# Optimization experiments

Hardware: AMD Instinct MI355X
Metric: run time of the kernel (lower is better)

Reference implementation:

```python
import jax, jax.numpy as jnp
import numpy as np

B, L, HID, NH, NB = 8, 1024, 512, 8, 8
HD = HID // NH


def setup_inputs() -> dict:
    key = jax.random.key(0)
    ks = jax.random.split(key, 12)
    s = 1.0 / np.sqrt(HID)
    x = jax.random.normal(ks[0], (B, L, HID), dtype=jnp.float32)
    time_bucket_matrix = jax.random.randint(ks[1], (B, L, L), 0, NB, dtype=jnp.int32)
    causal_mask = jnp.triu(jnp.ones((L, L), dtype=bool), k=1)  # True = masked (future)
    lens = jax.random.randint(ks[2], (B,), (7 * L) // 8, L + 1)
    padding_mask = jnp.arange(L)[None, :] >= lens[:, None]  # True = pad
    return {
        "x": x,
        "time_bucket_matrix": time_bucket_matrix,
        "causal_mask": causal_mask,
        "padding_mask": padding_mask,
        "Wq": jax.random.uniform(ks[3], (HID, HID), jnp.float32, -s, s),
        "bq": jnp.zeros((HID,), jnp.float32),
        "Wk": jax.random.uniform(ks[4], (HID, HID), jnp.float32, -s, s),
        "bk": jnp.zeros((HID,), jnp.float32),
        "Wv": jax.random.uniform(ks[5], (HID, HID), jnp.float32, -s, s),
        "bv": jnp.zeros((HID,), jnp.float32),
        "Wo": jax.random.uniform(ks[6], (HID, HID), jnp.float32, -s, s),
        "bo": jnp.zeros((HID,), jnp.float32),
        "time_emb": jax.random.normal(ks[7], (NB, NH), dtype=jnp.float32),
    }


def reference(x, time_bucket_matrix, causal_mask, padding_mask,
              Wq, bq, Wk, bk, Wv, bv, Wo, bo, time_emb):
    Bb, Ll, H = x.shape
    def heads(t):
        return t.reshape(Bb, Ll, NH, HD).transpose(0, 2, 1, 3)  # [B,NH,L,HD]
    q = heads(x @ Wq.T + bq)
    k = heads(x @ Wk.T + bk)
    v = heads(x @ Wv.T + bv)
    scores = jnp.einsum("bhqd,bhkd->bhqk", q, k) / jnp.sqrt(jnp.float32(HD))
    # per-(i,j) time-bucket bias: [B,L,L] -> [B,L,L,NH] -> [B,NH,L,L]
    t_bias = time_emb[time_bucket_matrix].transpose(0, 3, 1, 2)
    scores = scores + t_bias
    scores = jnp.where(causal_mask[None, None, :, :], -1e9, scores)
    scores = jnp.where(padding_mask[:, None, None, :], -1e9, scores)  # key pad
    w = jax.nn.softmax(scores, axis=-1)
    w = jnp.where(padding_mask[:, None, :, None], 0.0, w)  # query pad
    out = jnp.einsum("bhqk,bhkd->bhqd", w, v).transpose(0, 2, 1, 3).reshape(Bb, Ll, H)
    return out @ Wo.T + bo
```

## Files before the change

kernel.cpp:

```cpp
#include <hip/hip_runtime.h>
#include <hip/hip_bf16.h>
#include <cstdint>

#define L_SEQ 1024
#define HID_DIM 512
#define N_HEADS 8
#define HEAD_DIM 64
#define BATCH 8

typedef __attribute__((ext_vector_type(8))) short bf16x8;
typedef __attribute__((ext_vector_type(4))) float f32x4;

__device__ __forceinline__ ushort f2bf(float v) {
  __hip_bfloat16 hb = __float2bfloat16(v);
  return *(ushort*)&hb;
}

__global__ __launch_bounds__(256)
void prep_convert(const float* __restrict__ x, const float* __restrict__ Wq,
                  const float* __restrict__ Wk, const float* __restrict__ Wv,
                  const float* __restrict__ Wo, ushort* __restrict__ dst) {
  const size_t gid = (size_t)blockIdx.x * 256 + threadIdx.x;
  const size_t e = gid * 8;
  const float* src;
  size_t loc;
  if (e < 4194304) {
    src = x; loc = e;
  } else {
    const size_t r = e - 4194304;
    const int wsel = (int)(r >> 18);
    loc = r & 262143;
    src = (wsel == 0) ? Wq : (wsel == 1) ? Wk : (wsel == 2) ? Wv : Wo;
  }
  float4 v0 = *(const float4*)(src + loc);
  float4 v1 = *(const float4*)(src + loc + 4);
  ushort u[8];
  u[0] = f2bf(v0.x); u[1] = f2bf(v0.y); u[2] = f2bf(v0.z); u[3] = f2bf(v0.w);
  u[4] = f2bf(v1.x); u[5] = f2bf(v1.y); u[6] = f2bf(v1.z); u[7] = f2bf(v1.w);
  *(uint4*)(dst + e) = *(uint4*)u;
}

__global__ __launch_bounds__(256)
void lens_kernel(const uint8_t* __restrict__ pm, int* __restrict__ lens) {
  __shared__ int flag;
  __shared__ int part[256];
  const int b = blockIdx.x, tid = threadIdx.x;
  if (tid == 0) flag = 0;
  __syncthreads();
  const unsigned* pw = (const unsigned*)pm;
  unsigned any = 0;
  for (int i = tid; i < 2048; i += 256) any |= (pw[i] > 1u);
  if (any) flag = 1;
  __syncthreads();
  int c = 0;
  if (flag) {
    unsigned v = pw[b * 256 + tid];
    c = (int)((v & 0xFFu) == 0) + (int)(((v >> 8) & 0xFFu) == 0) +
        (int)(((v >> 16) & 0xFFu) == 0) + (int)(((v >> 24) & 0xFFu) == 0);
  } else {
    const int* pi = (const int*)pm;
    c = (int)(pi[b * 1024 + tid * 4 + 0] == 0) + (int)(pi[b * 1024 + tid * 4 + 1] == 0) +
        (int)(pi[b * 1024 + tid * 4 + 2] == 0) + (int)(pi[b * 1024 + tid * 4 + 3] == 0);
  }
  part[tid] = c;
  __syncthreads();
  for (int s = 128; s > 0; s >>= 1) {
    if (tid < s) part[tid] += part[tid + s];
    __syncthreads();
  }
  if (tid == 0) lens[b] = part[0];
}

__global__ __launch_bounds__(256, 3)
void qkv_lds(const ushort* __restrict__ xb, const ushort* __restrict__ wqb,
             const ushort* __restrict__ wkb, const ushort* __restrict__ wvb,
             const float* __restrict__ bq, const float* __restrict__ bk,
             const float* __restrict__ bv, ushort* __restrict__ qb,
             ushort* __restrict__ kb, ushort* __restrict__ vT) {
  __shared__ char lds[2][20480];
  const int tid = threadIdx.x;
  const int w = tid >> 6, lane = tid & 63;
  const int l15 = lane & 15, g = lane >> 4;
  const int z = blockIdx.z;
  const ushort* A = (z == 2) ? wvb : xb;
  const ushort* B = (z == 0) ? wqb : (z == 1) ? wkb : xb;
  const float* bias = (z == 0) ? bq : (z == 1) ? bk : bv;
  const int M0 = ((z == 2) ? blockIdx.y : blockIdx.x) * 128;
  const int N0 = ((z == 2) ? blockIdx.x : blockIdx.y) * 128;

  const int sr = tid >> 2, sc = tid & 3;
  const ushort* Ag = A + (size_t)(M0 + sr) * 512 + sc * 8;
  const ushort* Bg = B + (size_t)(N0 + sr) * 512 + sc * 8;
  const int wro = sr * 80 + sc * 16;
  uint4 sa0, sa1, sb0, sb1;

#define QSTAGE_LOAD(kc_)                                      \
  sa0 = *(const uint4*)(Ag + (kc_) * 32);                     \
  sa1 = *(const uint4*)(Ag + (size_t)64 * 512 + (kc_) * 32);  \
  sb0 = *(const uint4*)(Bg + (kc_) * 32);                     \
  sb1 = *(const uint4*)(Bg + (size_t)64 * 512 + (kc_) * 32);
#define QSTAGE_WRITE(buf)                                     \
  *(uint4*)&(buf)[wro] = sa0;                                 \
  *(uint4*)&(buf)[wro + 64 * 80] = sa1;                       \
  *(uint4*)&(buf)[10240 + wro] = sb0;                         \
  *(uint4*)&(buf)[10240 + wro + 64 * 80] = sb1;

  const int wm = w >> 1, wn = w & 1;
  const int aro = (wm * 64 + l15) * 80 + g * 16;
  const int bro = 10240 + (wn * 64 + l15) * 80 + g * 16;

  f32x4 acc[4][4];
#pragma unroll
  for (int i = 0; i < 4; ++i)
#pragma unroll
    for (int j = 0; j < 4; ++j) acc[i][j] = (f32x4){0.f, 0.f, 0.f, 0.f};

  QSTAGE_LOAD(0);
  QSTAGE_WRITE(lds[0]);
  __syncthreads();
  int cur = 0;
#pragma unroll 1
  for (int kc = 0; kc < 16; ++kc) {
    if (kc + 1 < 16) { QSTAGE_LOAD(kc + 1); }
    bf16x8 av[4], bv[4];
#pragma unroll
    for (int t = 0; t < 4; ++t) {
      av[t] = *(const bf16x8*)&lds[cur][aro + t * 1280];
      bv[t] = *(const bf16x8*)&lds[cur][bro + t * 1280];
    }
    __builtin_amdgcn_s_setprio(1);
#pragma unroll
    for (int i = 0; i < 4; ++i)
#pragma unroll
      for (int j = 0; j < 4; ++j)
        acc[i][j] = __builtin_amdgcn_mfma_f32_16x16x32_bf16(av[i], bv[j], acc[i][j], 0, 0, 0);
    __builtin_amdgcn_s_setprio(0);
    if (kc + 1 < 16) { QSTAGE_WRITE(lds[cur ^ 1]); }
    __syncthreads();
    cur ^= 1;
  }
#undef QSTAGE_LOAD
#undef QSTAGE_WRITE

  const int M0w = M0 + wm * 64, N0w = N0 + wn * 64;
  if (z < 2) {
    ushort* out = (z == 0) ? qb : kb;
    float bn[4];
#pragma unroll
    for (int nt = 0; nt < 4; ++nt) bn[nt] = bias[N0w + nt * 16 + l15];
#pragma unroll
    for (int mt = 0; mt < 4; ++mt)
#pragma unroll
      for (int nt = 0; nt < 4; ++nt)
#pragma unroll
        for (int r = 0; r < 4; ++r) {
          const int m = M0w + mt * 16 + 4 * g + r;
          const int n = N0w + nt * 16 + l15;
          out[(size_t)m * 512 + n] = f2bf(acc[mt][nt][r] + bn[nt]);
        }
  } else {
#pragma unroll
    for (int mt = 0; mt < 4; ++mt)
#pragma unroll
      for (int r = 0; r < 4; ++r) {
        const int m = M0w + mt * 16 + 4 * g + r;
        const float bm = bias[m];
#pragma unroll
        for (int nt = 0; nt < 4; ++nt) {
          const int tok = N0w + nt * 16 + l15;
          const size_t off = ((size_t)((tok >> 10) * 512 + m)) * 1024 + (tok & 1023);
          vT[off] = f2bf(acc[mt][nt][r] + bm);
        }
      }
  }
}

__global__ __launch_bounds__(256, 3)
void out_lds(const ushort* __restrict__ A, const ushort* __restrict__ B,
             const float* __restrict__ bias, float* __restrict__ out) {
  __shared__ char lds[2][15360];
  const int tid = threadIdx.x;
  const int w = tid >> 6, lane = tid & 63;
  const int l15 = lane & 15, g = lane >> 4;
  const int M0 = blockIdx.x * 64, N0 = blockIdx.y * 128;

  const int sr = tid >> 2, sc = tid & 3;
  const ushort* Ag = A + (size_t)(M0 + sr) * 512 + sc * 8;
  const ushort* Bg = B + (size_t)(N0 + sr) * 512 + sc * 8;
  const int wro = sr * 80 + sc * 16;
  uint4 sa0, sb0, sb1;

#define OSTAGE_LOAD(kc_)                                      \
  sa0 = *(const uint4*)(Ag + (kc_) * 32);                     \
  sb0 = *(const uint4*)(Bg + (kc_) * 32);                     \
  sb1 = *(const uint4*)(Bg + (size_t)64 * 512 + (kc_) * 32);
#define OSTAGE_WRITE(buf)                                     \
  *(uint4*)&(buf)[wro] = sa0;                                 \
  *(uint4*)&(buf)[5120 + wro] = sb0;                          \
  *(uint4*)&(buf)[5120 + wro + 64 * 80] = sb1;

  const int wm = w >> 1, wn = w & 1;
  const int aro = (wm * 32 + l15) * 80 + g * 16;
  const int bro = 5120 + (wn * 64 + l15) * 80 + g * 16;

  f32x4 acc[2][4];
#pragma unroll
  for (int i = 0; i < 2; ++i)
#pragma unroll
    for (int j = 0; j < 4; ++j) acc[i][j] = (f32x4){0.f, 0.f, 0.f, 0.f};

  OSTAGE_LOAD(0);
  OSTAGE_WRITE(lds[0]);
  __syncthreads();
  int cur = 0;
#pragma unroll 1
  for (int kc = 0; kc < 16; ++kc) {
    if (kc + 1 < 16) { OSTAGE_LOAD(kc + 1); }
    bf16x8 av[2], bv[4];
#pragma unroll
    for (int t = 0; t < 2; ++t) av[t] = *(const bf16x8*)&lds[cur][aro + t * 1280];
#pragma unroll
    for (int t = 0; t < 4; ++t) bv[t] = *(const bf16x8*)&lds[cur][bro + t * 1280];
    __builtin_amdgcn_s_setprio(1);
#pragma unroll
    for (int i = 0; i < 2; ++i)
#pragma unroll
      for (int j = 0; j < 4; ++j)
        acc[i][j] = __builtin_amdgcn_mfma_f32_16x16x32_bf16(av[i], bv[j], acc[i][j], 0, 0, 0);
    __builtin_amdgcn_s_setprio(0);
    if (kc + 1 < 16) { OSTAGE_WRITE(lds[cur ^ 1]); }
    __syncthreads();
    cur ^= 1;
  }
#undef OSTAGE_LOAD
#undef OSTAGE_WRITE

  const int M0w = M0 + wm * 32, N0w = N0 + wn * 64;
  float bn[4];
#pragma unroll
  for (int nt = 0; nt < 4; ++nt) bn[nt] = bias[N0w + nt * 16 + l15];
#pragma unroll
  for (int mt = 0; mt < 2; ++mt)
#pragma unroll
    for (int nt = 0; nt < 4; ++nt)
#pragma unroll
      for (int r = 0; r < 4; ++r) {
        const int m = M0w + mt * 16 + 4 * g + r;
        const int n = N0w + nt * 16 + l15;
        out[(size_t)m * 512 + n] = acc[mt][nt][r] + bn[nt];
      }
}

__global__ __launch_bounds__(256, 2)
void attn_mfma(const ushort* __restrict__ qb, const ushort* __restrict__ kb,
               const ushort* __restrict__ vT, const int* __restrict__ tbm,
               const float* __restrict__ temb, const int* __restrict__ lens,
               ushort* __restrict__ ab) {
  __shared__ char kv[2][16384];
  __shared__ char pbuf[4][2048];
  const int tid = threadIdx.x;
  const int w = tid >> 6;
  const int lane = tid & 63;
  const int l15 = lane & 15, g = lane >> 4;
  const int b = blockIdx.x, h = blockIdx.y;
  const int qg = 15 - blockIdx.z;
  const int len = lens[b];
  const int qbase = qg * 64 + 16 * w;

  const float te_src = temb[(lane & 7) * N_HEADS + h] * 1.44269504f;

  const int r0 = tid >> 3, c0 = tid & 7;
  const size_t kgrow = (size_t)(b * L_SEQ) * HID_DIM + h * HEAD_DIM + c0 * 8;
  const size_t vgrow = (size_t)((b * 8 + h) * 64 + r0) * L_SEQ + c0 * 8;
  const int so0 = (tid * 16) ^ ((r0 & 7) << 4);
  const int so1 = so0 + 4096;
  uint4 skA, skB, svA, svB;

#define STAGE_LOAD(kc_)                                                      \
  skA = *(const uint4*)(kb + kgrow + (size_t)((kc_) + r0) * HID_DIM);        \
  skB = *(const uint4*)(kb + kgrow + (size_t)((kc_) + r0 + 32) * HID_DIM);   \
  svA = *(const uint4*)(vT + vgrow + (kc_));                                 \
  svB = *(const uint4*)(vT + vgrow + 32 * L_SEQ + (kc_));

#define STAGE_WRITE(dst)                                                     \
  *(uint4*)&(dst)[so0] = skA;                                                \
  *(uint4*)&(dst)[so1] = skB;                                                \
  *(uint4*)&(dst)[8192 + so0] = svA;                                         \
  *(uint4*)&(dst)[8192 + so1] = svB;

  bf16x8 qf[2];
  {
    const ushort* qr = qb + (size_t)(b * L_SEQ + qbase + l15) * HID_DIM + h * HEAD_DIM + 8 * g;
    qf[0] = *(const bf16x8*)(qr);
    qf[1] = *(const bf16x8*)(qr + 32);
  }

  f32x4 O[4];
#pragma unroll
  for (int ct = 0; ct < 4; ++ct) O[ct] = (f32x4){0.f, 0.f, 0.f, 0.f};
  float ssum[4] = {0.f, 0.f, 0.f, 0.f};
  int tb_[4][4];

  const int lenc = (len - 1) >> 6;
  const int nch = (qg * 64 < len) ? ((qg < lenc ? qg : lenc) + 1) : 0;
  const int* tbq = tbm + (size_t)(b * L_SEQ + qbase) * L_SEQ;

  if (nch > 0) {
    STAGE_LOAD(0);
    STAGE_WRITE(kv[0]);
  }
  __syncthreads();

  int cur = 0;
#pragma unroll 1
  for (int c = 0; c < nch; ++c) {
    const int kc = c * 64;
#pragma unroll
    for (int kt = 0; kt < 4; ++kt)
#pragma unroll
      for (int r = 0; r < 4; ++r)
        tb_[kt][r] = tbq[(size_t)(4 * g + r) * L_SEQ + kc + 16 * kt + l15];
    if (c + 1 < nch) { STAGE_LOAD(kc + 64); }

    bf16x8 kf[4][2];
#pragma unroll
    for (int kt = 0; kt < 4; ++kt)
#pragma unroll
      for (int db = 0; db < 2; ++db) {
        const int off = ((2048 * kt + 128 * l15 + 16 * (g + 4 * db)) ^ ((l15 & 7) << 4));
        kf[kt][db] = *(const bf16x8*)&kv[cur][off];
      }
    f32x4 s[4];
    __builtin_amdgcn_s_setprio(1);
#pragma unroll
    for (int kt = 0; kt < 4; ++kt) {
      s[kt] = (f32x4){0.f, 0.f, 0.f, 0.f};
      s[kt] = __builtin_amdgcn_mfma_f32_16x16x32_bf16(qf[0], kf[kt][0], s[kt], 0, 0, 0);
      s[kt] = __builtin_amdgcn_mfma_f32_16x16x32_bf16(qf[1], kf[kt][1], s[kt], 0, 0, 0);
    }
    __builtin_amdgcn_s_setprio(0);

    bf16x8 vf[2][4];
#pragma unroll
    for (int kblk = 0; kblk < 2; ++kblk)
#pragma unroll
      for (int ct = 0; ct < 4; ++ct) {
        const int off = 8192 + ((2048 * ct + 128 * l15 + 16 * (4 * kblk + g)) ^ ((l15 & 7) << 4));
        vf[kblk][ct] = *(const bf16x8*)&kv[cur][off];
      }

#pragma unroll
    for (int kt = 0; kt < 4; ++kt) {
      const int kg = kc + 16 * kt + l15;
#pragma unroll
      for (int r = 0; r < 4; ++r) {
        const int lr = 4 * g + r;
        const int qgr = qbase + lr;
        const float te2 = __int_as_float(
            __builtin_amdgcn_ds_bpermute(tb_[kt][r] << 2, __float_as_int(te_src)));
        float pp = exp2f(fmaf(s[kt][r], 0.18033688f, te2));
        pp = (kg <= qgr && qgr < len) ? pp : 0.0f;
        ssum[r] += pp;
        const int off = ((lr * 128 + (16 * kt + l15) * 2) ^ ((lr & 7) << 4));
        *(ushort*)&pbuf[w][off] = f2bf(pp);
      }
    }

#pragma unroll
    for (int kblk = 0; kblk < 2; ++kblk) {
      const int off = ((l15 * 128 + kblk * 64 + 16 * g) ^ ((l15 & 7) << 4));
      const bf16x8 pf = *(const bf16x8*)(&pbuf[w][off]);
      __builtin_amdgcn_s_setprio(1);
#pragma unroll
      for (int ct = 0; ct < 4; ++ct)
        O[ct] = __builtin_amdgcn_mfma_f32_16x16x32_bf16(pf, vf[kblk][ct], O[ct], 0, 0, 0);
      __builtin_amdgcn_s_setprio(0);
    }

    if (c + 1 < nch) { STAGE_WRITE(kv[cur ^ 1]); }
    __syncthreads();
    cur ^= 1;
  }
#undef STAGE_LOAD
#undef STAGE_WRITE

#pragma unroll
  for (int m = 1; m <= 8; m <<= 1) {
#pragma unroll
    for (int r = 0; r < 4; ++r) ssum[r] += __shfl_xor(ssum[r], m, 64);
  }
#pragma unroll
  for (int ct = 0; ct < 4; ++ct)
#pragma unroll
    for (int r = 0; r < 4; ++r) {
      const int qgr = qbase + 4 * g + r;
      const float inv = (qgr < len && nch > 0) ? 1.0f / ssum[r] : 0.0f;
      ab[(size_t)(b * L_SEQ + qgr) * HID_DIM + h * HEAD_DIM + 16 * ct + l15] =
          f2bf(O[ct][r] * inv);
    }
}

extern "C" void kernel_launch(void* const* d_in, const int* in_sizes, int n_in,
                              void* d_out, int out_size, void* d_ws, size_t ws_size,
                              hipStream_t stream) {
  const float* x    = (const float*)d_in[0];
  const int*   tbm  = (const int*)d_in[1];
  const uint8_t* pm = (const uint8_t*)d_in[3];
  const float* Wq = (const float*)d_in[4];
  const float* bq = (const float*)d_in[5];
  const float* Wk = (const float*)d_in[6];
  const float* bk = (const float*)d_in[7];
  const float* Wv = (const float*)d_in[8];
  const float* bv = (const float*)d_in[9];
  const float* Wo = (const float*)d_in[10];
  const float* bo = (const float*)d_in[11];
  const float* temb = (const float*)d_in[12];
  float* out = (float*)d_out;

  const size_t NTOK = (size_t)BATCH * L_SEQ * HID_DIM;
  const size_t NW = 262144;
  ushort* ab  = (ushort*)d_ws;
  ushort* xb  = ab + NTOK;
  ushort* wqb = xb + NTOK;
  ushort* wkb = wqb + NW;
  ushort* wvb = wkb + NW;
  ushort* wob = wvb + NW;
  ushort* qb  = wob + NW;
  ushort* kb  = qb + NTOK;
  ushort* vT  = kb + NTOK;
  int* lens   = (int*)(vT + NTOK);

  prep_convert<<<2560, 256, 0, stream>>>(x, Wq, Wk, Wv, Wo, xb);
  lens_kernel<<<8, 256, 0, stream>>>(pm, lens);
  qkv_lds<<<dim3(64, 4, 3), 256, 0, stream>>>(xb, wqb, wkb, wvb, bq, bk, bv, qb, kb, vT);
  attn_mfma<<<dim3(8, 8, 16), 256, 0, stream>>>(qb, kb, vT, tbm, temb, lens, ab);
  out_lds<<<dim3(128, 4), 256, 0, stream>>>(ab, wob, bo, out);
}
```

Measured before the change: 79.91 us.

## Fuse fp32-to-bf16 conversion into GEMM loaders and split long attention query tiles

Removes the separate prep_convert pass by having the QKV and output GEMMs load fp32 inputs and weights and convert to bf16 while staging into LDS. The attention grid grows from 16 to 24 z-slices: the eight longest causal query tiles are each split into two key-range halves that write unnormalized partial outputs and row sums. A new merge kernel adds the halves and normalizes them. This is meant to balance the causal workload across blocks and drop one kernel launch plus a round trip through memory, at the cost of doubled fp32 global reads in the GEMMs and extra partial-buffer traffic. The split does not rescale by a running max, so it is only correct if the attention kernel uses a fixed softmax offset.

```diff
diff --git a/kernel.cpp b/kernel.cpp
--- a/kernel.cpp
+++ b/kernel.cpp
@@ -16,28 +16,11 @@
   return *(ushort*)&hb;
 }
 
-__global__ __launch_bounds__(256)
-void prep_convert(const float* __restrict__ x, const float* __restrict__ Wq,
-                  const float* __restrict__ Wk, const float* __restrict__ Wv,
-                  const float* __restrict__ Wo, ushort* __restrict__ dst) {
-  const size_t gid = (size_t)blockIdx.x * 256 + threadIdx.x;
-  const size_t e = gid * 8;
-  const float* src;
-  size_t loc;
-  if (e < 4194304) {
-    src = x; loc = e;
-  } else {
-    const size_t r = e - 4194304;
-    const int wsel = (int)(r >> 18);
-    loc = r & 262143;
-    src = (wsel == 0) ? Wq : (wsel == 1) ? Wk : (wsel == 2) ? Wv : Wo;
-  }
-  float4 v0 = *(const float4*)(src + loc);
-  float4 v1 = *(const float4*)(src + loc + 4);
+__device__ __forceinline__ uint4 cvt8(const float4 a, const float4 b) {
   ushort u[8];
-  u[0] = f2bf(v0.x); u[1] = f2bf(v0.y); u[2] = f2bf(v0.z); u[3] = f2bf(v0.w);
-  u[4] = f2bf(v1.x); u[5] = f2bf(v1.y); u[6] = f2bf(v1.z); u[7] = f2bf(v1.w);
-  *(uint4*)(dst + e) = *(uint4*)u;
+  u[0] = f2bf(a.x); u[1] = f2bf(a.y); u[2] = f2bf(a.z); u[3] = f2bf(a.w);
+  u[4] = f2bf(b.x); u[5] = f2bf(b.y); u[6] = f2bf(b.z); u[7] = f2bf(b.w);
+  return *(uint4*)u;
 }
 
 __global__ __launch_bounds__(256)
@@ -72,8 +55,8 @@
 }
 
 __global__ __launch_bounds__(256, 3)
-void qkv_lds(const ushort* __restrict__ xb, const ushort* __restrict__ wqb,
-             const ushort* __restrict__ wkb, const ushort* __restrict__ wvb,
+void qkv_lds(const float* __restrict__ x, const float* __restrict__ Wq,
+             const float* __restrict__ Wk, const float* __restrict__ Wv,
              const float* __restrict__ bq, const float* __restrict__ bk,
              const float* __restrict__ bv, ushort* __restrict__ qb,
              ushort* __restrict__ kb, ushort* __restrict__ vT) {
@@ -82,28 +65,32 @@
   const int w = tid >> 6, lane = tid & 63;
   const int l15 = lane & 15, g = lane >> 4;
   const int z = blockIdx.z;
-  const ushort* A = (z == 2) ? wvb : xb;
-  const ushort* B = (z == 0) ? wqb : (z == 1) ? wkb : xb;
+  const float* A = (z == 2) ? Wv : x;
+  const float* B = (z == 0) ? Wq : (z == 1) ? Wk : x;
   const float* bias = (z == 0) ? bq : (z == 1) ? bk : bv;
   const int M0 = ((z == 2) ? blockIdx.y : blockIdx.x) * 128;
   const int N0 = ((z == 2) ? blockIdx.x : blockIdx.y) * 128;
 
   const int sr = tid >> 2, sc = tid & 3;
-  const ushort* Ag = A + (size_t)(M0 + sr) * 512 + sc * 8;
-  const ushort* Bg = B + (size_t)(N0 + sr) * 512 + sc * 8;
+  const float* Ag = A + (size_t)(M0 + sr) * 512 + sc * 8;
+  const float* Bg = B + (size_t)(N0 + sr) * 512 + sc * 8;
   const int wro = sr * 80 + sc * 16;
-  uint4 sa0, sa1, sb0, sb1;
-
-#define QSTAGE_LOAD(kc_)                                      \
-  sa0 = *(const uint4*)(Ag + (kc_) * 32);                     \
-  sa1 = *(const uint4*)(Ag + (size_t)64 * 512 + (kc_) * 32);  \
-  sb0 = *(const uint4*)(Bg + (kc_) * 32);                     \
-  sb1 = *(const uint4*)(Bg + (size_t)64 * 512 + (kc_) * 32);
-#define QSTAGE_WRITE(buf)                                     \
-  *(uint4*)&(buf)[wro] = sa0;                                 \
-  *(uint4*)&(buf)[wro + 64 * 80] = sa1;                       \
-  *(uint4*)&(buf)[10240 + wro] = sb0;                         \
-  *(uint4*)&(buf)[10240 + wro + 64 * 80] = sb1;
+  float4 a00, a01, a10, a11, b00, b01, b10, b11;
+
+#define QSTAGE_LOAD(kc_)                                           \
+  a00 = *(const float4*)(Ag + (kc_) * 32);                         \
+  a01 = *(const float4*)(Ag + (kc_) * 32 + 4);                     \
+  a10 = *(const float4*)(Ag + (size_t)64 * 512 + (kc_) * 32);      \
+  a11 = *(const float4*)(Ag + (size_t)64 * 512 + (kc_) * 32 + 4);  \
+  b00 = *(const float4*)(Bg + (kc_) * 32);                         \
+  b01 = *(const float4*)(Bg + (kc_) * 32 + 4);                     \
+  b10 = *(const float4*)(Bg + (size_t)64 * 512 + (kc_) * 32);      \
+  b11 = *(const float4*)(Bg + (size_t)64 * 512 + (kc_) * 32 + 4);
+#define QSTAGE_WRITE(buf)                                          \
+  *(uint4*)&(buf)[wro] = cvt8(a00, a01);                           \
+  *(uint4*)&(buf)[wro + 64 * 80] = cvt8(a10, a11);                 \
+  *(uint4*)&(buf)[10240 + wro] = cvt8(b00, b01);                   \
+  *(uint4*)&(buf)[10240 + wro + 64 * 80] = cvt8(b10, b11);
 
   const int wm = w >> 1, wn = w & 1;
   const int aro = (wm * 64 + l15) * 80 + g * 16;
@@ -176,7 +163,7 @@
 }
 
 __global__ __launch_bounds__(256, 3)
-void out_lds(const ushort* __restrict__ A, const ushort* __restrict__ B,
+void out_lds(const ushort* __restrict__ A, const float* __restrict__ B,
              const float* __restrict__ bias, float* __restrict__ out) {
   __shared__ char lds[2][15360];
   const int tid = threadIdx.x;
@@ -186,18 +173,21 @@
 
   const int sr = tid >> 2, sc = tid & 3;
   const ushort* Ag = A + (size_t)(M0 + sr) * 512 + sc * 8;
-  const ushort* Bg = B + (size_t)(N0 + sr) * 512 + sc * 8;
+  const float* Bg = B + (size_t)(N0 + sr) * 512 + sc * 8;
   const int wro = sr * 80 + sc * 16;
-  uint4 sa0, sb0, sb1;
-
-#define OSTAGE_LOAD(kc_)                                      \
-  sa0 = *(const uint4*)(Ag + (kc_) * 32);                     \
-  sb0 = *(const uint4*)(Bg + (kc_) * 32);                     \
-  sb1 = *(const uint4*)(Bg + (size_t)64 * 512 + (kc_) * 32);
-#define OSTAGE_WRITE(buf)                                     \
-  *(uint4*)&(buf)[wro] = sa0;                                 \
-  *(uint4*)&(buf)[5120 + wro] = sb0;                          \
-  *(uint4*)&(buf)[5120 + wro + 64 * 80] = sb1;
+  uint4 sa0;
+  float4 b00, b01, b10, b11;
+
+#define OSTAGE_LOAD(kc_)                                           \
+  sa0 = *(const uint4*)(Ag + (kc_) * 32);                          \
+  b00 = *(const float4*)(Bg + (kc_) * 32);                         \
+  b01 = *(const float4*)(Bg + (kc_) * 32 + 4);                     \
+  b10 = *(const float4*)(Bg + (size_t)64 * 512 + (kc_) * 32);      \
+  b11 = *(const float4*)(Bg + (size_t)64 * 512 + (kc_) * 32 + 4);
+#define OSTAGE_WRITE(buf)                                          \
+  *(uint4*)&(buf)[wro] = sa0;                                      \
+  *(uint4*)&(buf)[5120 + wro] = cvt8(b00, b01);                    \
+  *(uint4*)&(buf)[5120 + wro + 64 * 80] = cvt8(b10, b11);
 
   const int wm = w >> 1, wn = w & 1;
   const int aro = (wm * 32 + l15) * 80 + g * 16;
@@ -255,7 +245,8 @@
 void attn_mfma(const ushort* __restrict__ qb, const ushort* __restrict__ kb,
                const ushort* __restrict__ vT, const int* __restrict__ tbm,
                const float* __restrict__ temb, const int* __restrict__ lens,
-               ushort* __restrict__ ab) {
+               ushort* __restrict__ ab, float* __restrict__ partO,
+               float* __restrict__ pssum) {
   __shared__ char kv[2][16384];
   __shared__ char pbuf[4][2048];
   const int tid = threadIdx.x;
@@ -263,15 +254,18 @@
   const int lane = tid & 63;
   const int l15 = lane & 15, g = lane >> 4;
   const int b = blockIdx.x, h = blockIdx.y;
-  const int qg = 15 - blockIdx.z;
+  const int z = blockIdx.z;
+  const bool split = (z < 16);
+  const int qg = split ? (15 - (z >> 1)) : (23 - z);
+  const int half = split ? (z & 1) : 0;
   const int len = lens[b];
   const int qbase = qg * 64 + 16 * w;
 
   const float te_src = temb[(lane & 7) * N_HEADS + h] * 1.44269504f;
 
-  const int r0 = tid >> 3, c0 = tid & 7;
-  const size_t kgrow = (size_t)(b * L_SEQ) * HID_DIM + h * HEAD_DIM + c0 * 8;
-  const size_t vgrow = (size_t)((b * 8 + h) * 64 + r0) * L_SEQ + c0 * 8;
+  const int r0 = tid >> 3, c0l = tid & 7;
+  const size_t kgrow = (size_t)(b * L_SEQ) * HID_DIM + h * HEAD_DIM + c0l * 8;
+  const size_t vgrow = (size_t)((b * 8 + h) * 64 + r0) * L_SEQ + c0l * 8;
   const int so0 = (tid * 16) ^ ((r0 & 7) << 4);
   const int so1 = so0 + 4096;
   uint4 skA, skB, svA, svB;
@@ -303,24 +297,30 @@
 
   const int lenc = (len - 1) >> 6;
   const int nch = (qg * 64 < len) ? ((qg < lenc ? qg : lenc) + 1) : 0;
+  int cbeg = 0, cend = nch;
+  if (split) {
+    const int mid = (nch + 1) >> 1;
+    cbeg = half ? mid : 0;
+    cend = half ? nch : mid;
+  }
   const int* tbq = tbm + (size_t)(b * L_SEQ + qbase) * L_SEQ;
 
-  if (nch > 0) {
-    STAGE_LOAD(0);
+  if (cend > cbeg) {
+    STAGE_LOAD(cbeg * 64);
     STAGE_WRITE(kv[0]);
   }
   __syncthreads();
 
   int cur = 0;
 #pragma unroll 1
-  for (int c = 0; c < nch; ++c) {
+  for (int c = cbeg; c < cend; ++c) {
     const int kc = c * 64;
 #pragma unroll
     for (int kt = 0; kt < 4; ++kt)
 #pragma unroll
       for (int r = 0; r < 4; ++r)
         tb_[kt][r] = tbq[(size_t)(4 * g + r) * L_SEQ + kc + 16 * kt + l15];
-    if (c + 1 < nch) { STAGE_LOAD(kc + 64); }
+    if (c + 1 < cend) { STAGE_LOAD(kc + 64); }
 
     bf16x8 kf[4][2];
 #pragma unroll
@@ -377,7 +377,7 @@
       __builtin_amdgcn_s_setprio(0);
     }
 
-    if (c + 1 < nch) { STAGE_WRITE(kv[cur ^ 1]); }
+    if (c + 1 < cend) { STAGE_WRITE(kv[cur ^ 1]); }
     __syncthreads();
     cur ^= 1;
   }
@@ -389,15 +389,54 @@
 #pragma unroll
     for (int r = 0; r < 4; ++r) ssum[r] += __shfl_xor(ssum[r], m, 64);
   }
-#pragma unroll
-  for (int ct = 0; ct < 4; ++ct)
-#pragma unroll
-    for (int r = 0; r < 4; ++r) {
-      const int qgr = qbase + 4 * g + r;
-      const float inv = (qgr < len && nch > 0) ? 1.0f / ssum[r] : 0.0f;
-      ab[(size_t)(b * L_SEQ + qgr) * HID_DIM + h * HEAD_DIM + 16 * ct + l15] =
-          f2bf(O[ct][r] * inv);
+
+  if (split) {
+    const int pidx = ((b * 8 + h) * 8 + (qg - 8));
+    float* po = partO + ((size_t)pidx * 2 + half) * 4096;
+    float* ps = pssum + ((size_t)pidx * 2 + half) * 64;
+#pragma unroll
+    for (int ct = 0; ct < 4; ++ct)
+#pragma unroll
+      for (int r = 0; r < 4; ++r)
+        po[(16 * w + 4 * g + r) * 64 + 16 * ct + l15] = O[ct][r];
+    if (l15 == 0) {
+#pragma unroll
+      for (int r = 0; r < 4; ++r) ps[16 * w + 4 * g + r] = ssum[r];
     }
+  } else {
+#pragma unroll
+    for (int ct = 0; ct < 4; ++ct)
+#pragma unroll
+      for (int r = 0; r < 4; ++r) {
+        const int qgr = qbase + 4 * g + r;
+        const float inv = (qgr < len && nch > 0) ? 1.0f / ssum[r] : 0.0f;
+        ab[(size_t)(b * L_SEQ + qgr) * HID_DIM + h * HEAD_DIM + 16 * ct + l15] =
+            f2bf(O[ct][r] * inv);
+      }
+  }
+}
+
+__global__ __launch_bounds__(256)
+void merge_kernel(const float* __restrict__ partO, const float* __restrict__ pssum,
+                  const int* __restrict__ lens, ushort* __restrict__ ab) {
+  const int b = blockIdx.x, h = blockIdx.y, j = blockIdx.z;
+  const int len = lens[b];
+  const int tid = threadIdx.x;
+  const int d = tid & 63, rbase = (tid >> 6) * 16;
+  const int pidx = (b * 8 + h) * 8 + j;
+  const float* p0 = partO + (size_t)pidx * 2 * 4096;
+  const float* p1 = p0 + 4096;
+  const float* s0 = pssum + (size_t)pidx * 2 * 64;
+  const float* s1 = s0 + 64;
+#pragma unroll
+  for (int i = 0; i < 16; ++i) {
+    const int row = rbase + i;
+    const int qgr = (8 + j) * 64 + row;
+    const float s = s0[row] + s1[row];
+    const float o = p0[row * 64 + d] + p1[row * 64 + d];
+    const float v = (qgr < len) ? o / s : 0.0f;
+    ab[(size_t)(b * L_SEQ + qgr) * HID_DIM + h * HEAD_DIM + d] = f2bf(v);
+  }
 }
 
 extern "C" void kernel_launch(void* const* d_in, const int* in_sizes, int n_in,
@@ -418,21 +457,17 @@
   float* out = (float*)d_out;
 
   const size_t NTOK = (size_t)BATCH * L_SEQ * HID_DIM;
-  const size_t NW = 262144;
   ushort* ab  = (ushort*)d_ws;
-  ushort* xb  = ab + NTOK;
-  ushort* wqb = xb + NTOK;
-  ushort* wkb = wqb + NW;
-  ushort* wvb = wkb + NW;
-  ushort* wob = wvb + NW;
-  ushort* qb  = wob + NW;
+  ushort* qb  = ab + NTOK;
   ushort* kb  = qb + NTOK;
   ushort* vT  = kb + NTOK;
   int* lens   = (int*)(vT + NTOK);
-
-  prep_convert<<<2560, 256, 0, stream>>>(x, Wq, Wk, Wv, Wo, xb);
+  float* partO = (float*)(lens + 64);
+  float* pssum = partO + (size_t)512 * 2 * 4096;
+
   lens_kernel<<<8, 256, 0, stream>>>(pm, lens);
-  qkv_lds<<<dim3(64, 4, 3), 256, 0, stream>>>(xb, wqb, wkb, wvb, bq, bk, bv, qb, kb, vT);
-  attn_mfma<<<dim3(8, 8, 16), 256, 0, stream>>>(qb, kb, vT, tbm, temb, lens, ab);
-  out_lds<<<dim3(128, 4), 256, 0, stream>>>(ab, wob, bo, out);
-}
+  qkv_lds<<<dim3(64, 4, 3), 256, 0, stream>>>(x, Wq, Wk, Wv, bq, bk, bv, qb, kb, vT);
+  attn_mfma<<<dim3(8, 8, 24), 256, 0, stream>>>(qb, kb, vT, tbm, temb, lens, ab, partO, pssum);
+  merge_kernel<<<dim3(8, 8, 8), 256, 0, stream>>>(partO, pssum, lens, ab);
+  out_lds<<<dim3(128, 4), 256, 0, stream>>>(ab, Wo, bo, out);
+}
```

Result: slower. 103.9 us (+30.0%).

## Prefetch time-bucket tiles one chunk ahead and skip fully masked causal subtiles

Applied to the files above, without the earlier changes.

The time-bucket index loads for the next key chunk are now issued a chunk ahead into alternating register sets, with the loop manually unrolled by two, so their global latency overlaps the current chunk's compute. In the diagonal chunk, QK MFMAs, exp work and PV MFMAs for 16-key and 32-key subtiles lying entirely above the causal diagonal are skipped, and the probability buffer is zeroed there instead. The cost is more live registers, which under the two-blocks-per-SM launch bound could cause spills, plus a larger unrolled body.

```diff
diff --git a/kernel.cpp b/kernel.cpp
--- a/kernel.cpp
+++ b/kernel.cpp
@@ -266,12 +266,13 @@
   const int qg = 15 - blockIdx.z;
   const int len = lens[b];
   const int qbase = qg * 64 + 16 * w;
+  const int qmax = qbase + 15;
 
   const float te_src = temb[(lane & 7) * N_HEADS + h] * 1.44269504f;
 
-  const int r0 = tid >> 3, c0 = tid & 7;
-  const size_t kgrow = (size_t)(b * L_SEQ) * HID_DIM + h * HEAD_DIM + c0 * 8;
-  const size_t vgrow = (size_t)((b * 8 + h) * 64 + r0) * L_SEQ + c0 * 8;
+  const int r0 = tid >> 3, c0l = tid & 7;
+  const size_t kgrow = (size_t)(b * L_SEQ) * HID_DIM + h * HEAD_DIM + c0l * 8;
+  const size_t vgrow = (size_t)((b * 8 + h) * 64 + r0) * L_SEQ + c0l * 8;
   const int so0 = (tid * 16) ^ ((r0 & 7) << 4);
   const int so1 = so0 + 4096;
   uint4 skA, skB, svA, svB;
@@ -299,90 +300,107 @@
 #pragma unroll
   for (int ct = 0; ct < 4; ++ct) O[ct] = (f32x4){0.f, 0.f, 0.f, 0.f};
   float ssum[4] = {0.f, 0.f, 0.f, 0.f};
-  int tb_[4][4];
 
   const int lenc = (len - 1) >> 6;
   const int nch = (qg * 64 < len) ? ((qg < lenc ? qg : lenc) + 1) : 0;
   const int* tbq = tbm + (size_t)(b * L_SEQ + qbase) * L_SEQ;
 
+#define LOAD_TB(dst, cc)                                                     \
+  {                                                                          \
+    const int* tb_p = tbq + (cc) * 64;                                       \
+    _Pragma("unroll") for (int kt = 0; kt < 4; ++kt)                         \
+      _Pragma("unroll") for (int r = 0; r < 4; ++r)                          \
+        dst[kt][r] = tb_p[(size_t)(4 * g + r) * L_SEQ + 16 * kt + l15];      \
+  }
+
+#define COMPUTE_CHUNK(tbv, c_)                                               \
+  {                                                                          \
+    const int kc = (c_) * 64;                                                \
+    bf16x8 kf[4][2];                                                         \
+    _Pragma("unroll") for (int kt = 0; kt < 4; ++kt)                         \
+      _Pragma("unroll") for (int db = 0; db < 2; ++db) {                     \
+        const int off = ((2048 * kt + 128 * l15 + 16 * (g + 4 * db)) ^ ((l15 & 7) << 4)); \
+        kf[kt][db] = *(const bf16x8*)&kv[cur][off];                          \
+      }                                                                      \
+    f32x4 s[4];                                                              \
+    __builtin_amdgcn_s_setprio(1);                                           \
+    _Pragma("unroll") for (int kt = 0; kt < 4; ++kt) {                       \
+      if (kc + 16 * kt <= qmax) {                                            \
+        s[kt] = (f32x4){0.f, 0.f, 0.f, 0.f};                                 \
+        s[kt] = __builtin_amdgcn_mfma_f32_16x16x32_bf16(qf[0], kf[kt][0], s[kt], 0, 0, 0); \
+        s[kt] = __builtin_amdgcn_mfma_f32_16x16x32_bf16(qf[1], kf[kt][1], s[kt], 0, 0, 0); \
+      }                                                                      \
+    }                                                                        \
+    __builtin_amdgcn_s_setprio(0);                                           \
+    bf16x8 vf[2][4];                                                         \
+    _Pragma("unroll") for (int kblk = 0; kblk < 2; ++kblk)                   \
+      _Pragma("unroll") for (int ct = 0; ct < 4; ++ct) {                     \
+        const int off = 8192 + ((2048 * ct + 128 * l15 + 16 * (4 * kblk + g)) ^ ((l15 & 7) << 4)); \
+        vf[kblk][ct] = *(const bf16x8*)&kv[cur][off];                        \
+      }                                                                      \
+    _Pragma("unroll") for (int kt = 0; kt < 4; ++kt) {                       \
+      const int kg = kc + 16 * kt + l15;                                     \
+      if (kc + 16 * kt <= qmax) {                                            \
+        _Pragma("unroll") for (int r = 0; r < 4; ++r) {                      \
+          const int lr = 4 * g + r;                                          \
+          const int qgr = qbase + lr;                                        \
+          const float te2 = __int_as_float(                                  \
+              __builtin_amdgcn_ds_bpermute(tbv[kt][r] << 2, __float_as_int(te_src))); \
+          float pp = exp2f(fmaf(s[kt][r], 0.18033688f, te2));                \
+          pp = (kg <= qgr && qgr < len) ? pp : 0.0f;                         \
+          ssum[r] += pp;                                                     \
+          const int off = ((lr * 128 + (16 * kt + l15) * 2) ^ ((lr & 7) << 4)); \
+          *(ushort*)&pbuf[w][off] = f2bf(pp);                                \
+        }                                                                    \
+      } else {                                                               \
+        _Pragma("unroll") for (int r = 0; r < 4; ++r) {                      \
+          const int lr = 4 * g + r;                                          \
+          const int off = ((lr * 128 + (16 * kt + l15) * 2) ^ ((lr & 7) << 4)); \
+          *(ushort*)&pbuf[w][off] = 0;                                       \
+        }                                                                    \
+      }                                                                      \
+    }                                                                        \
+    _Pragma("unroll") for (int kblk = 0; kblk < 2; ++kblk) {                 \
+      if (kc + 32 * kblk <= qmax) {                                          \
+        const int off = ((l15 * 128 + kblk * 64 + 16 * g) ^ ((l15 & 7) << 4)); \
+        const bf16x8 pf = *(const bf16x8*)(&pbuf[w][off]);                   \
+        __builtin_amdgcn_s_setprio(1);                                       \
+        _Pragma("unroll") for (int ct = 0; ct < 4; ++ct)                     \
+          O[ct] = __builtin_amdgcn_mfma_f32_16x16x32_bf16(pf, vf[kblk][ct], O[ct], 0, 0, 0); \
+        __builtin_amdgcn_s_setprio(0);                                       \
+      }                                                                      \
+    }                                                                        \
+  }
+
+  int tbA_[4][4], tbB_[4][4];
   if (nch > 0) {
     STAGE_LOAD(0);
     STAGE_WRITE(kv[0]);
+    LOAD_TB(tbA_, 0);
   }
   __syncthreads();
 
   int cur = 0;
-#pragma unroll 1
-  for (int c = 0; c < nch; ++c) {
-    const int kc = c * 64;
-#pragma unroll
-    for (int kt = 0; kt < 4; ++kt)
-#pragma unroll
-      for (int r = 0; r < 4; ++r)
-        tb_[kt][r] = tbq[(size_t)(4 * g + r) * L_SEQ + kc + 16 * kt + l15];
-    if (c + 1 < nch) { STAGE_LOAD(kc + 64); }
-
-    bf16x8 kf[4][2];
-#pragma unroll
-    for (int kt = 0; kt < 4; ++kt)
-#pragma unroll
-      for (int db = 0; db < 2; ++db) {
-        const int off = ((2048 * kt + 128 * l15 + 16 * (g + 4 * db)) ^ ((l15 & 7) << 4));
-        kf[kt][db] = *(const bf16x8*)&kv[cur][off];
-      }
-    f32x4 s[4];
-    __builtin_amdgcn_s_setprio(1);
-#pragma unroll
-    for (int kt = 0; kt < 4; ++kt) {
-      s[kt] = (f32x4){0.f, 0.f, 0.f, 0.f};
-      s[kt] = __builtin_amdgcn_mfma_f32_16x16x32_bf16(qf[0], kf[kt][0], s[kt], 0, 0, 0);
-      s[kt] = __builtin_amdgcn_mfma_f32_16x16x32_bf16(qf[1], kf[kt][1], s[kt], 0, 0, 0);
-    }
-    __builtin_amdgcn_s_setprio(0);
-
-    bf16x8 vf[2][4];
-#pragma unroll
-    for (int kblk = 0; kblk < 2; ++kblk)
-#pragma unroll
-      for (int ct = 0; ct < 4; ++ct) {
-        const int off = 8192 + ((2048 * ct + 128 * l15 + 16 * (4 * kblk + g)) ^ ((l15 & 7) << 4));
-        vf[kblk][ct] = *(const bf16x8*)&kv[cur][off];
-      }
-
-#pragma unroll
-    for (int kt = 0; kt < 4; ++kt) {
-      const int kg = kc + 16 * kt + l15;
-#pragma unroll
-      for (int r = 0; r < 4; ++r) {
-        const int lr = 4 * g + r;
-        const int qgr = qbase + lr;
-        const float te2 = __int_as_float(
-            __builtin_amdgcn_ds_bpermute(tb_[kt][r] << 2, __float_as_int(te_src)));
-        float pp = exp2f(fmaf(s[kt][r], 0.18033688f, te2));
-        pp = (kg <= qgr && qgr < len) ? pp : 0.0f;
-        ssum[r] += pp;
-        const int off = ((lr * 128 + (16 * kt + l15) * 2) ^ ((lr & 7) << 4));
-        *(ushort*)&pbuf[w][off] = f2bf(pp);
-      }
-    }
-
-#pragma unroll
-    for (int kblk = 0; kblk < 2; ++kblk) {
-      const int off = ((l15 * 128 + kblk * 64 + 16 * g) ^ ((l15 & 7) << 4));
-      const bf16x8 pf = *(const bf16x8*)(&pbuf[w][off]);
-      __builtin_amdgcn_s_setprio(1);
-#pragma unroll
-      for (int ct = 0; ct < 4; ++ct)
-        O[ct] = __builtin_amdgcn_mfma_f32_16x16x32_bf16(pf, vf[kblk][ct], O[ct], 0, 0, 0);
-      __builtin_amdgcn_s_setprio(0);
-    }
-
+  int c = 0;
+  while (c < nch) {
+    if (c + 1 < nch) { LOAD_TB(tbB_, c + 1); STAGE_LOAD((c + 1) * 64); }
+    COMPUTE_CHUNK(tbA_, c);
     if (c + 1 < nch) { STAGE_WRITE(kv[cur ^ 1]); }
     __syncthreads();
     cur ^= 1;
+    ++c;
+    if (c >= nch) break;
+    if (c + 1 < nch) { LOAD_TB(tbA_, c + 1); STAGE_LOAD((c + 1) * 64); }
+    COMPUTE_CHUNK(tbB_, c);
+    if (c + 1 < nch) { STAGE_WRITE(kv[cur ^ 1]); }
+    __syncthreads();
+    cur ^= 1;
+    ++c;
   }
 #undef STAGE_LOAD
 #undef STAGE_WRITE
+#undef LOAD_TB
+#undef COMPUTE_CHUNK
 
 #pragma unroll
   for (int m = 1; m <= 8; m <<= 1) {
```

New measurement: 87.97 us. +10.1%, slower.
